# Optimization experiments

Measured on AMD Instinct MI355X. Metric: run time of the kernel, lower is better.

## Reference

```python
import jax, jax.numpy as jnp
import numpy as np

N, NW, M, H, C = 16384, 512, 32, 8, 16
T_SEG, N_SIG = 512, 3


def _forward(query_feats, key_feats, value_feats, query_table, key_table,
             value_table, table_offsets, win_indices, table_idx):
    # gather voxels into windows: [nW, M, H, C]
    q = query_feats[win_indices]
    k = key_feats[win_indices]
    v = value_feats[win_indices]
    # base attention coefficients: [nW, H, M, M]
    logits = jnp.einsum('wihc,wjhc->whij', q, k)
    n_sig = table_idx.shape[-1]
    for s in range(n_sig):  # fixed, small signal loop (xyz cRSE)
        idx_s = table_offsets[s] + table_idx[..., s]      # [nW, M, M]
        tq = query_table[idx_s]                            # [nW, M, M, H, C]
        tk = key_table[idx_s]
        logits = logits + jnp.einsum('wihc,wijhc->whij', q, tq) \
                        + jnp.einsum('wjhc,wijhc->whij', k, tk)
    # max-stabilized exp (cal_max_coffs + self_attn_forward)
    rmax = jnp.max(logits, axis=-1, keepdims=True)
    ecoff = jnp.exp(logits - rmax)                         # [nW, H, M, M]
    sum_coffs = jnp.sum(ecoff, axis=-1)                    # [nW, H, M]
    raw = jnp.einsum('whij,wjhc->wihc', ecoff, v)          # [nW, M, H, C]
    for s in range(n_sig):
        idx_s = table_offsets[s] + table_idx[..., s]
        tv = value_table[idx_s]
        raw = raw + jnp.einsum('whij,wijhc->wihc', ecoff, tv)
    norm = raw / jnp.transpose(sum_coffs, (0, 2, 1))[..., None]
    # scatter windows back to voxel order (win_indices is a permutation)
    out = jnp.zeros_like(query_feats).at[win_indices.reshape(-1)].set(
        norm.reshape(-1, norm.shape[-2], norm.shape[-1]))
    return out


def setup_inputs() -> dict:
    key = jax.random.key(0)
    ks = jax.random.split(key, 9)
    feats = lambda k: jax.random.normal(k, (N, H, C), dtype=jnp.float32)
    table = lambda k: 0.02 * jax.random.normal(k, (N_SIG * T_SEG, H, C), dtype=jnp.float32)
    win_indices = jax.random.permutation(ks[6], N).reshape(NW, M).astype(jnp.int32)
    table_idx = jax.random.randint(ks[7], (NW, M, M, N_SIG), 0, T_SEG, dtype=jnp.int32)
    table_offsets = (jnp.arange(N_SIG, dtype=jnp.int32) * T_SEG)
    return {
        'query_feats': feats(ks[0]), 'key_feats': feats(ks[1]), 'value_feats': feats(ks[2]),
        'query_table': table(ks[3]), 'key_table': table(ks[4]), 'value_table': table(ks[5]),
        'table_offsets': table_offsets, 'win_indices': win_indices, 'table_idx': table_idx,
    }


def reference(query_feats, key_feats, value_feats, query_table, key_table,
              value_table, table_offsets, win_indices, table_idx):
    return _forward(query_feats, key_feats, value_feats, query_table, key_table,
                    value_table, table_offsets, win_indices, table_idx)
```

## Files before the change

kernel.cpp:

```cpp
#include <hip/hip_runtime.h>

namespace {
constexpr int NWIN = 512;
constexpr int M    = 32;
constexpr int H    = 8;
constexpr int C    = 16;
constexpr int NSIG = 3;
constexpr int HC   = H * C;
}

__device__ __forceinline__ float dot4(const float4& a, const float4& b) {
  return a.x * b.x + a.y * b.y + a.z * b.z + a.w * b.w;
}
__device__ __forceinline__ const float4* f4p(const float* p) {
  return reinterpret_cast<const float4*>(p);
}

__global__ __launch_bounds__(256, 2)
void win_attn(const float* __restrict__ qf, const float* __restrict__ kf,
              const float* __restrict__ vf, const float* __restrict__ qt,
              const float* __restrict__ kt, const float* __restrict__ vt,
              const int* __restrict__ toff, const int* __restrict__ widx,
              const int* __restrict__ tidx, float* __restrict__ out)
{
  const int w = blockIdx.x;
  const int t = threadIdx.x;
  const int h = t >> 5;
  const int i = t & 31;

  __shared__ float k_lds[M][HC];
  __shared__ float v_lds[M][HC];
  __shared__ int   tid_lds[M * NSIG * M];
  __shared__ int   vox_lds[M];
  __shared__ int   off_lds[NSIG];

  if (t < M)    vox_lds[t] = widx[w * M + t];
  if (t < NSIG) off_lds[t] = toff[t];
  __syncthreads();

  #pragma unroll
  for (int r = 0; r < 4; ++r) {
    const int flat = t + 256 * r;
    const int j    = flat >> 5;
    const int f4i  = (flat & 31) * 4;
    const int vox  = vox_lds[j];
    *reinterpret_cast<float4*>(&k_lds[j][f4i]) = *f4p(kf + vox * HC + f4i);
    *reinterpret_cast<float4*>(&v_lds[j][f4i]) = *f4p(vf + vox * HC + f4i);
  }
  #pragma unroll
  for (int r = 0; r < 12; ++r) {
    const int g   = t + 256 * r;
    const int ii  = g / 96;
    const int rem = g - ii * 96;
    const int jj  = rem / 3;
    const int ss  = rem - jj * 3;
    tid_lds[(jj * NSIG + ss) * M + ii] = tidx[w * (M * M * NSIG) + g];
  }

  const int vox_i = vox_lds[i];
  const float* qrow = qf + vox_i * HC + h * C;
  const float4 q0 = *f4p(qrow + 0),  q1 = *f4p(qrow + 4),
               q2 = *f4p(qrow + 8),  q3 = *f4p(qrow + 12);
  const int offs[NSIG] = { off_lds[0], off_lds[1], off_lds[2] };
  __syncthreads();

  float lg[M];
  #pragma unroll
  for (int j = 0; j < M; ++j) {
    const float* krow = &k_lds[j][h * C];
    const float4 k0 = *f4p(krow + 0),  k1 = *f4p(krow + 4),
                 k2 = *f4p(krow + 8),  k3 = *f4p(krow + 12);
    float acc = dot4(q0, k0) + dot4(q1, k1) + dot4(q2, k2) + dot4(q3, k3);
    #pragma unroll
    for (int s = 0; s < NSIG; ++s) {
      const int row = offs[s] + tid_lds[(j * NSIG + s) * M + i];
      const float* tqr = qt + row * HC + h * C;
      const float4 a0 = *f4p(tqr + 0),  a1 = *f4p(tqr + 4),
                   a2 = *f4p(tqr + 8),  a3 = *f4p(tqr + 12);
      acc += dot4(q0, a0) + dot4(q1, a1) + dot4(q2, a2) + dot4(q3, a3);
      const float* tkr = kt + row * HC + h * C;
      const float4 b0 = *f4p(tkr + 0),  b1 = *f4p(tkr + 4),
                   b2 = *f4p(tkr + 8),  b3 = *f4p(tkr + 12);
      acc += dot4(k0, b0) + dot4(k1, b1) + dot4(k2, b2) + dot4(k3, b3);
    }
    lg[j] = acc;
  }

  float m = lg[0];
  #pragma unroll
  for (int j = 1; j < M; ++j) m = fmaxf(m, lg[j]);
  float ssum = 0.f;
  #pragma unroll
  for (int j = 0; j < M; ++j) { lg[j] = expf(lg[j] - m); ssum += lg[j]; }

  float oacc[C];
  #pragma unroll
  for (int c = 0; c < C; ++c) oacc[c] = 0.f;
  #pragma unroll
  for (int j = 0; j < M; ++j) {
    const float e = lg[j];
    const float* vrow = &v_lds[j][h * C];
    #pragma unroll
    for (int c4 = 0; c4 < 4; ++c4) {
      const float4 vv = *f4p(vrow + 4 * c4);
      oacc[4 * c4 + 0] += e * vv.x;
      oacc[4 * c4 + 1] += e * vv.y;
      oacc[4 * c4 + 2] += e * vv.z;
      oacc[4 * c4 + 3] += e * vv.w;
    }
    #pragma unroll
    for (int s = 0; s < NSIG; ++s) {
      const int row = offs[s] + tid_lds[(j * NSIG + s) * M + i];
      const float* tvr = vt + row * HC + h * C;
      #pragma unroll
      for (int c4 = 0; c4 < 4; ++c4) {
        const float4 tv = *f4p(tvr + 4 * c4);
        oacc[4 * c4 + 0] += e * tv.x;
        oacc[4 * c4 + 1] += e * tv.y;
        oacc[4 * c4 + 2] += e * tv.z;
        oacc[4 * c4 + 3] += e * tv.w;
      }
    }
  }

  const float inv = 1.0f / ssum;
  float* orow = out + vox_i * HC + h * C;
  #pragma unroll
  for (int c4 = 0; c4 < 4; ++c4) {
    float4 o;
    o.x = oacc[4 * c4 + 0] * inv;
    o.y = oacc[4 * c4 + 1] * inv;
    o.z = oacc[4 * c4 + 2] * inv;
    o.w = oacc[4 * c4 + 3] * inv;
    *reinterpret_cast<float4*>(orow + 4 * c4) = o;
  }
}

extern "C" void kernel_launch(void* const* d_in, const int* in_sizes, int n_in,
                              void* d_out, int out_size, void* d_ws, size_t ws_size,
                              hipStream_t stream) {
  (void)in_sizes; (void)n_in; (void)d_ws; (void)ws_size; (void)out_size;
  const float* qf  = (const float*)d_in[0];
  const float* kf  = (const float*)d_in[1];
  const float* vf  = (const float*)d_in[2];
  const float* qt  = (const float*)d_in[3];
  const float* kt  = (const float*)d_in[4];
  const float* vt  = (const float*)d_in[5];
  const int*  toff = (const int*)d_in[6];
  const int*  widx = (const int*)d_in[7];
  const int*  tidx = (const int*)d_in[8];
  float* out = (float*)d_out;
  win_attn<<<NWIN, 256, 0, stream>>>(qf, kf, vf, qt, kt, vt, toff, widx, tidx, out);
}
```

Before: 356.4 us.

## Split heads across two blocks and channels across wave halves

Each window is now handled by two blocks of four heads each, and within a head the 16 channels are split between two 32-lane halves of a 64-wide wavefront. The partial logits are combined with a cross-half shuffle. This halves the per-thread register state (q/k vectors, output accumulators) so launch bounds can request more resident blocks, and doubles the grid to 1024 blocks. The cost is that table indices are loaded into LDS twice per window, plus the extra shuffles.

```diff
diff --git a/kernel.cpp b/kernel.cpp
--- a/kernel.cpp
+++ b/kernel.cpp
@@ -7,6 +7,8 @@
 constexpr int C    = 16;
 constexpr int NSIG = 3;
 constexpr int HC   = H * C;
+constexpr int HB   = 4;
+constexpr int HBC  = HB * C;
 }
 
 __device__ __forceinline__ float dot4(const float4& a, const float4& b) {
@@ -16,20 +18,24 @@
   return reinterpret_cast<const float4*>(p);
 }
 
-__global__ __launch_bounds__(256, 2)
+__global__ __launch_bounds__(256, 4)
 void win_attn(const float* __restrict__ qf, const float* __restrict__ kf,
               const float* __restrict__ vf, const float* __restrict__ qt,
               const float* __restrict__ kt, const float* __restrict__ vt,
               const int* __restrict__ toff, const int* __restrict__ widx,
               const int* __restrict__ tidx, float* __restrict__ out)
 {
-  const int w = blockIdx.x;
-  const int t = threadIdx.x;
-  const int h = t >> 5;
-  const int i = t & 31;
+  const int w  = blockIdx.x >> 1;
+  const int hb = (blockIdx.x & 1) * HB;
+  const int t  = threadIdx.x;
+  const int hl = t >> 6;
+  const int ch = (t >> 5) & 1;
+  const int i  = t & 31;
+  const int h  = hb + hl;
+  const int cb = ch * 8;
 
-  __shared__ float k_lds[M][HC];
-  __shared__ float v_lds[M][HC];
+  __shared__ float k_lds[M][HBC];
+  __shared__ float v_lds[M][HBC];
   __shared__ int   tid_lds[M * NSIG * M];
   __shared__ int   vox_lds[M];
   __shared__ int   off_lds[NSIG];
@@ -39,13 +45,13 @@
   __syncthreads();
 
   #pragma unroll
-  for (int r = 0; r < 4; ++r) {
+  for (int r = 0; r < 2; ++r) {
     const int flat = t + 256 * r;
-    const int j    = flat >> 5;
-    const int f4i  = (flat & 31) * 4;
-    const int vox  = vox_lds[j];
-    *reinterpret_cast<float4*>(&k_lds[j][f4i]) = *f4p(kf + vox * HC + f4i);
-    *reinterpret_cast<float4*>(&v_lds[j][f4i]) = *f4p(vf + vox * HC + f4i);
+    const int j    = flat >> 4;
+    const int f4i  = (flat & 15) * 4;
+    const int goff = vox_lds[j] * HC + hb * C + f4i;
+    *reinterpret_cast<float4*>(&k_lds[j][f4i]) = *f4p(kf + goff);
+    *reinterpret_cast<float4*>(&v_lds[j][f4i]) = *f4p(vf + goff);
   }
   #pragma unroll
   for (int r = 0; r < 12; ++r) {
@@ -58,31 +64,26 @@
   }
 
   const int vox_i = vox_lds[i];
-  const float* qrow = qf + vox_i * HC + h * C;
-  const float4 q0 = *f4p(qrow + 0),  q1 = *f4p(qrow + 4),
-               q2 = *f4p(qrow + 8),  q3 = *f4p(qrow + 12);
+  const float* qrow = qf + vox_i * HC + h * C + cb;
+  const float4 q0 = f4p(qrow)[0], q1 = f4p(qrow)[1];
   const int offs[NSIG] = { off_lds[0], off_lds[1], off_lds[2] };
   __syncthreads();
 
   float lg[M];
   #pragma unroll
   for (int j = 0; j < M; ++j) {
-    const float* krow = &k_lds[j][h * C];
-    const float4 k0 = *f4p(krow + 0),  k1 = *f4p(krow + 4),
-                 k2 = *f4p(krow + 8),  k3 = *f4p(krow + 12);
-    float acc = dot4(q0, k0) + dot4(q1, k1) + dot4(q2, k2) + dot4(q3, k3);
+    const float* krow = &k_lds[j][hl * C + cb];
+    const float4 k0 = f4p(krow)[0], k1 = f4p(krow)[1];
+    float acc = dot4(q0, k0) + dot4(q1, k1);
     #pragma unroll
     for (int s = 0; s < NSIG; ++s) {
       const int row = offs[s] + tid_lds[(j * NSIG + s) * M + i];
-      const float* tqr = qt + row * HC + h * C;
-      const float4 a0 = *f4p(tqr + 0),  a1 = *f4p(tqr + 4),
-                   a2 = *f4p(tqr + 8),  a3 = *f4p(tqr + 12);
-      acc += dot4(q0, a0) + dot4(q1, a1) + dot4(q2, a2) + dot4(q3, a3);
-      const float* tkr = kt + row * HC + h * C;
-      const float4 b0 = *f4p(tkr + 0),  b1 = *f4p(tkr + 4),
-                   b2 = *f4p(tkr + 8),  b3 = *f4p(tkr + 12);
-      acc += dot4(k0, b0) + dot4(k1, b1) + dot4(k2, b2) + dot4(k3, b3);
+      const float* tqr = qt + row * HC + h * C + cb;
+      acc += dot4(q0, f4p(tqr)[0]) + dot4(q1, f4p(tqr)[1]);
+      const float* tkr = kt + row * HC + h * C + cb;
+      acc += dot4(k0, f4p(tkr)[0]) + dot4(k1, f4p(tkr)[1]);
     }
+    acc += __shfl_xor(acc, 32);
     lg[j] = acc;
   }
 
@@ -93,16 +94,16 @@
   #pragma unroll
   for (int j = 0; j < M; ++j) { lg[j] = expf(lg[j] - m); ssum += lg[j]; }
 
-  float oacc[C];
+  float oacc[8];
   #pragma unroll
-  for (int c = 0; c < C; ++c) oacc[c] = 0.f;
+  for (int c = 0; c < 8; ++c) oacc[c] = 0.f;
   #pragma unroll
   for (int j = 0; j < M; ++j) {
     const float e = lg[j];
-    const float* vrow = &v_lds[j][h * C];
+    const float* vrow = &v_lds[j][hl * C + cb];
     #pragma unroll
-    for (int c4 = 0; c4 < 4; ++c4) {
-      const float4 vv = *f4p(vrow + 4 * c4);
+    for (int c4 = 0; c4 < 2; ++c4) {
+      const float4 vv = f4p(vrow)[c4];
       oacc[4 * c4 + 0] += e * vv.x;
       oacc[4 * c4 + 1] += e * vv.y;
       oacc[4 * c4 + 2] += e * vv.z;
@@ -111,10 +112,10 @@
     #pragma unroll
     for (int s = 0; s < NSIG; ++s) {
       const int row = offs[s] + tid_lds[(j * NSIG + s) * M + i];
-      const float* tvr = vt + row * HC + h * C;
+      const float* tvr = vt + row * HC + h * C + cb;
       #pragma unroll
-      for (int c4 = 0; c4 < 4; ++c4) {
-        const float4 tv = *f4p(tvr + 4 * c4);
+      for (int c4 = 0; c4 < 2; ++c4) {
+        const float4 tv = f4p(tvr)[c4];
         oacc[4 * c4 + 0] += e * tv.x;
         oacc[4 * c4 + 1] += e * tv.y;
         oacc[4 * c4 + 2] += e * tv.z;
@@ -124,9 +125,9 @@
   }
 
   const float inv = 1.0f / ssum;
-  float* orow = out + vox_i * HC + h * C;
+  float* orow = out + vox_i * HC + h * C + cb;
   #pragma unroll
-  for (int c4 = 0; c4 < 4; ++c4) {
+  for (int c4 = 0; c4 < 2; ++c4) {
     float4 o;
     o.x = oacc[4 * c4 + 0] * inv;
     o.y = oacc[4 * c4 + 1] * inv;
@@ -150,5 +151,5 @@
   const int*  widx = (const int*)d_in[7];
   const int*  tidx = (const int*)d_in[8];
   float* out = (float*)d_out;
-  win_attn<<<NWIN, 256, 0, stream>>>(qf, kf, vf, qt, kt, vt, toff, widx, tidx, out);
+  win_attn<<<NWIN * 2, 256, 0, stream>>>(qf, kf, vf, qt, kt, vt, toff, widx, tidx, out);
 }
```

Result: slower. 413.6 us (+16.0%).
